# Performance work log

Hardware: AMD Instinct MI355X
Metric: run time of the kernel (lower is better)

## Reference

```python
import jax, jax.numpy as jnp
import numpy as np

# Gemma2-9B layer config
HID = 3584
H = 16          # query heads
KV = 8          # kv heads
G = H // KV     # GQA group size
DH = 256        # head dim
INTER = 14336
WINDOW = 1024   # sliding window size
LOGIT_CAP = 50.0
SCALING = 256.0 ** -0.5   # query_pre_attn_scalar ** -0.5
EPS = 1e-6
ROPE_BASE = 10000.0
B, S = 2, 2048


def gemma_rmsnorm(x, w, eps=EPS):
    # Gemma RMSNorm: fp32 compute, scale by (1 + w)
    xf = x.astype(jnp.float32)
    var = jnp.mean(xf * xf, axis=-1, keepdims=True)
    return (xf * jax.lax.rsqrt(var + eps) * (1.0 + w.astype(jnp.float32))).astype(x.dtype)


def apply_rope(pos, x):
    # neox-style rotary embedding; x: [B, S, n_heads, DH], pos: [B, S]
    half = DH // 2
    inv_freq = 1.0 / (ROPE_BASE ** (jnp.arange(0, half, dtype=jnp.float32) / half * 1.0))
    inv_freq = 1.0 / (ROPE_BASE ** (jnp.arange(0, DH, 2, dtype=jnp.float32) / DH))
    ang = pos.astype(jnp.float32)[..., None] * inv_freq          # [B, S, half]
    cos = jnp.cos(ang)[:, :, None, :]                            # [B, S, 1, half]
    sin = jnp.sin(ang)[:, :, None, :]
    x1, x2 = x[..., :half], x[..., half:]
    return jnp.concatenate([x1 * cos - x2 * sin, x2 * cos + x1 * sin], axis=-1).astype(x.dtype)


def setup_inputs() -> dict:
    key = jax.random.key(0)
    ks = jax.random.split(key, 12)
    s = 0.02
    inp = {
        "hidden_states": jax.random.normal(ks[0], (B, S, HID), dtype=jnp.float32),
        "positions": jnp.tile(jnp.arange(S, dtype=jnp.int32)[None, :], (B, 1)),
        "in_ln_w": jax.random.normal(ks[1], (HID,), dtype=jnp.float32) * s,
        "post_attn_ln_w": jax.random.normal(ks[2], (HID,), dtype=jnp.float32) * s,
        "pre_ff_ln_w": jax.random.normal(ks[3], (HID,), dtype=jnp.float32) * s,
        "post_ff_ln_w": jax.random.normal(ks[4], (HID,), dtype=jnp.float32) * s,
        "q_w": jax.random.normal(ks[5], (HID, H * DH), dtype=jnp.float32) * s,
        "k_w": jax.random.normal(ks[6], (HID, KV * DH), dtype=jnp.float32) * s,
        "v_w": jax.random.normal(ks[7], (HID, KV * DH), dtype=jnp.float32) * s,
        "o_w": jax.random.normal(ks[8], (H * DH, HID), dtype=jnp.float32) * s,
        "gate_w": jax.random.normal(ks[9], (HID, INTER), dtype=jnp.float32) * s,
        "up_w": jax.random.normal(ks[10], (HID, INTER), dtype=jnp.float32) * s,
        "down_w": jax.random.normal(ks[11], (INTER, HID), dtype=jnp.float32) * s,
    }
    return inp


def _decoder_layer(hidden_states, positions, in_ln_w, post_attn_ln_w, pre_ff_ln_w,
                   post_ff_ln_w, q_w, k_w, v_w, o_w, gate_w, up_w, down_w):
    # residual is None path
    residual = hidden_states
    x = gemma_rmsnorm(hidden_states, in_ln_w)

    # ---- attention ----
    q = (x @ q_w).reshape(B, S, H, DH)
    k = (x @ k_w).reshape(B, S, KV, DH)
    v = (x @ v_w).reshape(B, S, KV, DH)
    q = apply_rope(positions, q)
    k = apply_rope(positions, k)
    kv_fused = jnp.stack([k, v], axis=0)  # paged KV-cache write, modeled densely

    qg = q.reshape(B, S, KV, G, DH)
    # scores: [B, KV, G, S(q), S(k)]
    scores = jnp.einsum('bsngd,btnd->bngst', qg, k) * SCALING
    scores = LOGIT_CAP * jnp.tanh(scores / LOGIT_CAP)  # logit softcapping
    i = jnp.arange(S)[:, None]
    j = jnp.arange(S)[None, :]
    mask = (j <= i) & (i - j < WINDOW)                 # causal + sliding window
    scores = jnp.where(mask, scores, jnp.finfo(scores.dtype).min)
    probs = jax.nn.softmax(scores, axis=-1)
    attn = jnp.einsum('bngst,btnd->bsngd', probs, v).reshape(B, S, H * DH)
    attn_out = attn @ o_w

    x = gemma_rmsnorm(attn_out, post_attn_ln_w)
    x = residual + x
    residual = x

    # ---- GeGLU MLP ----
    x = gemma_rmsnorm(x, pre_ff_ln_w)
    inter = (x @ up_w) * jax.nn.gelu(x @ gate_w)
    x = inter @ down_w
    x = gemma_rmsnorm(x, post_ff_ln_w)
    return x, residual, kv_fused


def reference(hidden_states, positions, in_ln_w, post_attn_ln_w, pre_ff_ln_w,
              post_ff_ln_w, q_w, k_w, v_w, o_w, gate_w, up_w, down_w):
    return _decoder_layer(hidden_states, positions, in_ln_w, post_attn_ln_w,
                          pre_ff_ln_w, post_ff_ln_w, q_w, k_w, v_w, o_w,
                          gate_w, up_w, down_w)
```

## Files before the change

kernel.cpp:

```cpp
#include <hip/hip_runtime.h>
#include <stdint.h>

typedef unsigned short ushortT;
typedef float f32x4 __attribute__((ext_vector_type(4)));
typedef short short8 __attribute__((ext_vector_type(8)));

#define HID 3584
#define NH 16
#define NKV 8
#define DH 256
#define SEQ 2048
#define NB 2
#define NTOK 4096
#define INTERDIM 14336
#define WINDOW 1024

__device__ __forceinline__ ushortT f2bf(float x) {
  union { float f; uint32_t u; } v; v.f = x;
  uint32_t r = v.u + 0x7fffu + ((v.u >> 16) & 1u);
  return (ushortT)(r >> 16);
}
__device__ __forceinline__ float bf2f(uint32_t b) {
  union { uint32_t u; float f; } v; v.u = b << 16;
  return v.f;
}
__device__ __forceinline__ void gll16(const void* g, void* l) {
  __builtin_amdgcn_global_load_lds((const __attribute__((address_space(1))) void*)g,
                                   (__attribute__((address_space(3))) void*)l, 16, 0, 0);
}
__device__ __forceinline__ void sbar() {
  asm volatile("" ::: "memory");
  __builtin_amdgcn_s_barrier();
  asm volatile("" ::: "memory");
}
__device__ __forceinline__ void vmdrain() {
  asm volatile("s_waitcnt vmcnt(0)" ::: "memory");
}

__global__ __launch_bounds__(256) void transpose_cvt(const float* __restrict__ in,
                                                     ushortT* __restrict__ out,
                                                     int in_rs, int out_rs) {
  __shared__ float tile[64][65];
  const int r0 = blockIdx.y * 64, c0 = blockIdx.x * 64;
  const int t = threadIdx.x, tc = (t & 15) * 4, tr = t >> 4;
#pragma unroll
  for (int p = 0; p < 4; ++p) {
    int r = tr + p * 16;
    float4 v = *(const float4*)&in[(size_t)(r0 + r) * in_rs + c0 + tc];
    tile[r][tc] = v.x; tile[r][tc + 1] = v.y; tile[r][tc + 2] = v.z; tile[r][tc + 3] = v.w;
  }
  __syncthreads();
#pragma unroll
  for (int p = 0; p < 4; ++p) {
    int r = tr + p * 16;
    ushort4 u;
    u.x = f2bf(tile[tc + 0][r]); u.y = f2bf(tile[tc + 1][r]);
    u.z = f2bf(tile[tc + 2][r]); u.w = f2bf(tile[tc + 3][r]);
    *(ushort4*)&out[(size_t)(c0 + r) * out_rs + r0 + tc] = u;
  }
}

__global__ __launch_bounds__(256) void vtrans(const float* __restrict__ vsrc,
                                              ushortT* __restrict__ vT) {
  __shared__ float tile[64][65];
  const int z = blockIdx.z, b = z >> 3, n = z & 7;
  const float* in = vsrc + (size_t)b * SEQ * (NKV * DH) + n * DH;
  ushortT* out = vT + (size_t)z * DH * SEQ;
  const int s0 = blockIdx.y * 64, d0 = blockIdx.x * 64;
  const int t = threadIdx.x, tc = (t & 15) * 4, tr = t >> 4;
#pragma unroll
  for (int p = 0; p < 4; ++p) {
    int r = tr + p * 16;
    float4 v = *(const float4*)&in[(size_t)(s0 + r) * (NKV * DH) + d0 + tc];
    tile[r][tc] = v.x; tile[r][tc + 1] = v.y; tile[r][tc + 2] = v.z; tile[r][tc + 3] = v.w;
  }
  __syncthreads();
#pragma unroll
  for (int p = 0; p < 4; ++p) {
    int r = tr + p * 16;
    ushort4 u;
    u.x = f2bf(tile[tc + 0][r]); u.y = f2bf(tile[tc + 1][r]);
    u.z = f2bf(tile[tc + 2][r]); u.w = f2bf(tile[tc + 3][r]);
    *(ushort4*)&out[(size_t)(d0 + r) * SEQ + s0 + tc] = u;
  }
}

__device__ __forceinline__ float block_sum448(float v, float* sb) {
#pragma unroll
  for (int o = 32; o; o >>= 1) v += __shfl_xor(v, o, 64);
  __syncthreads();
  if ((threadIdx.x & 63) == 0) sb[threadIdx.x >> 6] = v;
  __syncthreads();
  float s = 0.f;
#pragma unroll
  for (int i = 0; i < 7; ++i) s += sb[i];
  return s;
}

__global__ __launch_bounds__(448) void rms_in(const float* __restrict__ in,
                                              const float* __restrict__ w,
                                              ushortT* __restrict__ out) {
  __shared__ float sb[8];
  const size_t row = blockIdx.x;
  const int c = threadIdx.x * 8;
  const float* p = in + row * HID + c;
  float4 a = *(const float4*)p, bq = *(const float4*)(p + 4);
  float v[8] = {a.x, a.y, a.z, a.w, bq.x, bq.y, bq.z, bq.w};
  float ssq = 0.f;
#pragma unroll
  for (int j = 0; j < 8; ++j) ssq += v[j] * v[j];
  float s = block_sum448(ssq, sb);
  float rs = rsqrtf(s * (1.0f / HID) + 1e-6f);
  uint32_t o[4];
#pragma unroll
  for (int j = 0; j < 4; ++j) {
    float r0 = v[2 * j] * rs * (1.f + w[c + 2 * j]);
    float r1 = v[2 * j + 1] * rs * (1.f + w[c + 2 * j + 1]);
    o[j] = (uint32_t)f2bf(r0) | ((uint32_t)f2bf(r1) << 16);
  }
  *(uint4*)(out + row * HID + c) = make_uint4(o[0], o[1], o[2], o[3]);
}

__global__ __launch_bounds__(448) void rms_add(const float* ao,
                                               const float* __restrict__ h,
                                               const float* __restrict__ w1,
                                               const float* __restrict__ w2,
                                               float* resid,
                                               ushortT* __restrict__ x2) {
  __shared__ float sb[8];
  const size_t row = blockIdx.x;
  const int c = threadIdx.x * 8;
  const float* p = ao + row * HID + c;
  float4 a = *(const float4*)p, bq = *(const float4*)(p + 4);
  float v[8] = {a.x, a.y, a.z, a.w, bq.x, bq.y, bq.z, bq.w};
  float ssq = 0.f;
#pragma unroll
  for (int j = 0; j < 8; ++j) ssq += v[j] * v[j];
  float s1 = block_sum448(ssq, sb);
  float rs1 = rsqrtf(s1 * (1.0f / HID) + 1e-6f);
  const float* hp = h + row * HID + c;
  float4 h0 = *(const float4*)hp, h1 = *(const float4*)(hp + 4);
  float hv[8] = {h0.x, h0.y, h0.z, h0.w, h1.x, h1.y, h1.z, h1.w};
  float r[8];
  float ssq2 = 0.f;
#pragma unroll
  for (int j = 0; j < 8; ++j) {
    r[j] = hv[j] + v[j] * rs1 * (1.f + w1[c + j]);
    ssq2 += r[j] * r[j];
  }
  float* rp = resid + row * HID + c;
  *(float4*)rp = make_float4(r[0], r[1], r[2], r[3]);
  *(float4*)(rp + 4) = make_float4(r[4], r[5], r[6], r[7]);
  float s2 = block_sum448(ssq2, sb);
  float rs2 = rsqrtf(s2 * (1.0f / HID) + 1e-6f);
  uint32_t o[4];
#pragma unroll
  for (int j = 0; j < 4; ++j) {
    float q0 = r[2 * j] * rs2 * (1.f + w2[c + 2 * j]);
    float q1 = r[2 * j + 1] * rs2 * (1.f + w2[c + 2 * j + 1]);
    o[j] = (uint32_t)f2bf(q0) | ((uint32_t)f2bf(q1) << 16);
  }
  *(uint4*)(x2 + row * HID + c) = make_uint4(o[0], o[1], o[2], o[3]);
}

__global__ __launch_bounds__(448) void rms_out(const float* in,
                                               const float* __restrict__ w,
                                               float* out) {
  __shared__ float sb[8];
  const size_t row = blockIdx.x;
  const int c = threadIdx.x * 8;
  const float* p = in + row * HID + c;
  float4 a = *(const float4*)p, bq = *(const float4*)(p + 4);
  float v[8] = {a.x, a.y, a.z, a.w, bq.x, bq.y, bq.z, bq.w};
  float ssq = 0.f;
#pragma unroll
  for (int j = 0; j < 8; ++j) ssq += v[j] * v[j];
  float s = block_sum448(ssq, sb);
  float rs = rsqrtf(s * (1.0f / HID) + 1e-6f);
  float* op = out + row * HID + c;
  float r[8];
#pragma unroll
  for (int j = 0; j < 8; ++j) r[j] = v[j] * rs * (1.f + w[c + j]);
  *(float4*)op = make_float4(r[0], r[1], r[2], r[3]);
  *(float4*)(op + 4) = make_float4(r[4], r[5], r[6], r[7]);
}

__global__ __launch_bounds__(128) void rope_q_k(const ushortT* __restrict__ qk,
                                                const int* __restrict__ pos,
                                                ushortT* __restrict__ qr) {
  const int s = blockIdx.x, h = blockIdx.y, b = blockIdx.z, i = threadIdx.x;
  float p = (float)pos[b * SEQ + s];
  float ang = p * exp2f(-(float)i * (13.287712379549449f / 128.f));
  float sn, cs;
  sincosf(ang, &sn, &cs);
  size_t ib = ((size_t)b * SEQ + s) * 6144 + (size_t)h * DH + i;
  float x1 = bf2f(qk[ib]), x2 = bf2f(qk[ib + 128]);
  size_t ob = (((size_t)b * NH + h) * SEQ + s) * DH + i;
  qr[ob] = f2bf(x1 * cs - x2 * sn);
  qr[ob + 128] = f2bf(x2 * cs + x1 * sn);
}

__global__ __launch_bounds__(128) void rope_k_k(const ushortT* __restrict__ qk,
                                                const int* __restrict__ pos,
                                                ushortT* __restrict__ kr,
                                                float* __restrict__ kv0) {
  const int s = blockIdx.x, n = blockIdx.y, b = blockIdx.z, i = threadIdx.x;
  float p = (float)pos[b * SEQ + s];
  float ang = p * exp2f(-(float)i * (13.287712379549449f / 128.f));
  float sn, cs;
  sincosf(ang, &sn, &cs);
  size_t ib = ((size_t)b * SEQ + s) * 6144 + 4096 + (size_t)n * DH + i;
  float x1 = bf2f(qk[ib]), x2 = bf2f(qk[ib + 128]);
  float o1 = x1 * cs - x2 * sn, o2 = x2 * cs + x1 * sn;
  size_t ob = (((size_t)b * NKV + n) * SEQ + s) * DH + i;
  kr[ob] = f2bf(o1);
  kr[ob + 128] = f2bf(o2);
  size_t kb = (((size_t)b * SEQ + s) * NKV + n) * DH + i;
  kv0[kb] = o1;
  kv0[kb + 128] = o2;
}

template <int OUTMODE>
__global__ __launch_bounds__(512) void gemm256(const ushortT* __restrict__ A, int lda,
                                               const ushortT* __restrict__ Bt, int ldb,
                                               void* C, const ushortT* G,
                                               int N, int K) {
  __shared__ ushortT lds[65536];
  char* lbase = (char*)lds;
  const int tid = threadIdx.x;
  const int nwg = gridDim.x * gridDim.y;
  const int lin = blockIdx.y * gridDim.x + blockIdx.x;
  const int cpx = nwg >> 3;
  const int lin2 = (lin & 7) * cpx + (lin >> 3);
  const int gy = gridDim.y;
  const int sq = lin2 / (gy * 16);
  const int rem = lin2 - sq * gy * 16;
  const int colq = rem / gy;
  const int bx = sq * 16 + colq;
  const int by = rem - colq * gy;
  const int m0 = by * 256, n0 = bx * 256;
  const int l = tid & 63, lr = l & 15, lg = l >> 4;
  const int wid = tid >> 6, wm2 = wid >> 2, wn4 = wid & 3;
  const int sr = tid >> 3, sc = tid & 7;

  f32x4 acc[8][4];
#pragma unroll
  for (int i = 0; i < 8; ++i)
#pragma unroll
    for (int j = 0; j < 4; ++j) acc[i][j] = (f32x4){0.f, 0.f, 0.f, 0.f};

  const int nt = K >> 6;
  const ushortT* Abase = A + (size_t)m0 * lda;
  const ushortT* Bbase = Bt + (size_t)n0 * ldb;

  auto stage_op = [&](const ushortT* gsrc, int ld, char* ldst) {
#pragma unroll
    for (int Li = 0; Li < 4; ++Li) {
      int r = Li * 64 + sr;
      gll16((const char*)(gsrc + (size_t)r * ld) + ((sc ^ (r & 7)) << 4),
            ldst + Li * 8192 + tid * 16);
    }
  };

  stage_op(Abase, lda, lbase);
  stage_op(Bbase, ldb, lbase + 32768);

  for (int t = 0; t < nt; ++t) {
    const int buf = t & 1;
    const char* Ab = lbase + buf * 65536 + wm2 * 16384;
    const char* Bb = lbase + buf * 65536 + 32768 + (wn4 >> 1) * 16384;
    short8 af[4][2], bfr[2][2];
#pragma unroll
    for (int q = 0; q < 4; ++q) {
      const int mh = q >> 1, nh = q & 1;
      if (q == 0) vmdrain();
      sbar();
      if (nh == 0) {
#pragma unroll
        for (int i = 0; i < 4; ++i) {
          int rA = mh * 64 + i * 16 + lr;
          int sw = rA & 7;
#pragma unroll
          for (int ks = 0; ks < 2; ++ks)
            af[i][ks] = *(const short8*)(Ab + rA * 128 + (((ks * 4 + lg) ^ sw) << 4));
        }
      }
#pragma unroll
      for (int j = 0; j < 2; ++j) {
        int rB = (wn4 & 1) * 64 + nh * 32 + j * 16 + lr;
        int sw = rB & 7;
#pragma unroll
        for (int ks = 0; ks < 2; ++ks)
          bfr[j][ks] = *(const short8*)(Bb + rB * 128 + (((ks * 4 + lg) ^ sw) << 4));
      }
      if (q == 0 && t + 1 < nt)
        stage_op(Abase + (size_t)(t + 1) * 64, lda, lbase + (buf ^ 1) * 65536);
      if (q == 1 && t + 1 < nt)
        stage_op(Bbase + (size_t)(t + 1) * 64, ldb, lbase + (buf ^ 1) * 65536 + 32768);
      __builtin_amdgcn_s_setprio(1);
#pragma unroll
      for (int i = 0; i < 4; ++i)
#pragma unroll
        for (int j = 0; j < 2; ++j)
#pragma unroll
          for (int ks = 0; ks < 2; ++ks)
            acc[mh * 4 + i][nh * 2 + j] = __builtin_amdgcn_mfma_f32_16x16x32_bf16(
                af[i][ks], bfr[j][ks], acc[mh * 4 + i][nh * 2 + j], 0, 0, 0);
      __builtin_amdgcn_s_setprio(0);
    }
  }
#pragma unroll
  for (int mi = 0; mi < 8; ++mi)
#pragma unroll
    for (int nj = 0; nj < 4; ++nj)
#pragma unroll
      for (int r = 0; r < 4; ++r) {
        size_t row = (size_t)(m0 + wm2 * 128 + mi * 16 + lg * 4 + r);
        size_t col = (size_t)(n0 + wn4 * 64 + nj * 16 + lr);
        size_t idx = row * N + col;
        if (OUTMODE == 0)
          ((float*)C)[idx] = acc[mi][nj][r];
        else if (OUTMODE == 1)
          ((ushortT*)C)[idx] = f2bf(acc[mi][nj][r]);
        else if (OUTMODE == 2)
          ((float*)C)[idx] += acc[mi][nj][r];
        else {
          float u = acc[mi][nj][r];
          float g = bf2f(G[idx]);
          float e = 0.5f * g * (1.f + tanhf(0.7978845608f * (g + 0.044715f * g * g * g)));
          ((ushortT*)C)[idx] = f2bf(u * e);
        }
      }
}

__global__ __launch_bounds__(256) void attn_fwd(const ushortT* __restrict__ Q,
                                                const ushortT* __restrict__ Kk,
                                                const ushortT* __restrict__ Vt,
                                                ushortT* __restrict__ Out) {
  __shared__ ushortT Kl[32 * 256];
  __shared__ ushortT Vl[256 * 32];
  __shared__ ushortT Pl[4][16 * 32];
  const int tid = threadIdx.x;
  const int w = tid >> 6, l = tid & 63, lr = l & 15, lg = l >> 4;
  const int h = blockIdx.y, b = blockIdx.z;
  const int n = h >> 1;
  const int qs = blockIdx.x * 64;
  const int sw = qs + w * 16;

  const ushortT* qp = Q + (((size_t)b * NH + h) * SEQ + (sw + lr)) * DH;
  short8 qf[8];
#pragma unroll
  for (int kk = 0; kk < 8; ++kk) qf[kk] = *(const short8*)(qp + kk * 32 + lg * 8);

  f32x4 acc[16];
#pragma unroll
  for (int i = 0; i < 16; ++i) acc[i] = (f32x4){0.f, 0.f, 0.f, 0.f};
  float m_s = -1e30f, l_s = 0.f;

  const ushortT* Kbase = Kk + ((size_t)b * NKV + n) * SEQ * DH;
  const ushortT* Vbase = Vt + ((size_t)b * NKV + n) * DH * SEQ;

  int tlo = qs - (WINDOW - 1);
  if (tlo < 0) tlo = 0;
  const int t0b = tlo & ~31;
  const int nt = (qs + 64 - t0b) >> 5;
  const int scol = sw + lr;

  for (int it = 0; it < nt; ++it) {
    const int t0 = t0b + it * 32;
    __syncthreads();
    {
      const int rowk = tid >> 5;
      const int cbk = (tid & 31) * 16;
#pragma unroll
      for (int c = 0; c < 4; ++c) {
        int row = c * 8 + rowk;
        int cbs = cbk ^ ((row & 7) << 4);
        gll16((const char*)(Kbase + (size_t)(t0 + row) * DH) + cbs, (char*)Kl + c * 4096 + tid * 16);
      }
      const int rowv = tid >> 2;
      const int cbv = (tid & 3) * 16;
#pragma unroll
      for (int c = 0; c < 4; ++c) {
        int row = c * 64 + rowv;
        int cbs = cbv ^ ((row & 3) << 4);
        gll16((const char*)(Vbase + (size_t)row * SEQ + t0) + cbs, (char*)Vl + c * 4096 + tid * 16);
      }
    }
    __syncthreads();
    f32x4 st[2];
#pragma unroll
    for (int tt = 0; tt < 2; ++tt) {
      f32x4 a = (f32x4){0.f, 0.f, 0.f, 0.f};
      const int krow = tt * 16 + lr;
      const char* kb = (const char*)Kl + krow * 512;
      const int swz = (krow & 7) << 4;
#pragma unroll
      for (int kk = 0; kk < 8; ++kk) {
        short8 kf = *(const short8*)(kb + ((kk * 64 + lg * 16) ^ swz));
        a = __builtin_amdgcn_mfma_f32_16x16x32_bf16(kf, qf[kk], a, 0, 0, 0);
      }
      st[tt] = a;
    }
    float pvv[8];
    float tmax = -1e30f;
#pragma unroll
    for (int tt = 0; tt < 2; ++tt)
#pragma unroll
      for (int r = 0; r < 4; ++r) {
        int t = t0 + tt * 16 + lg * 4 + r;
        float x = st[tt][r] * 0.0625f;
        x = 50.f * tanhf(x * 0.02f);
        bool ok = (t <= scol) && (scol - t < WINDOW);
        x = ok ? x : -1e30f;
        pvv[tt * 4 + r] = x;
        tmax = fmaxf(tmax, x);
      }
    tmax = fmaxf(tmax, __shfl_xor(tmax, 16, 64));
    tmax = fmaxf(tmax, __shfl_xor(tmax, 32, 64));
    float mnew = fmaxf(m_s, tmax);
    float fsc = __expf(m_s - mnew);
    m_s = mnew;
    float tsum = 0.f;
#pragma unroll
    for (int i = 0; i < 8; ++i) {
      pvv[i] = __expf(pvv[i] - mnew);
      tsum += pvv[i];
    }
    tsum += __shfl_xor(tsum, 16, 64);
    tsum += __shfl_xor(tsum, 32, 64);
    l_s = l_s * fsc + tsum;
    {
      char* pb = (char*)&Pl[w][0] + lr * 64;
      const int pswz = (lr & 3) << 4;
#pragma unroll
      for (int tt = 0; tt < 2; ++tt) {
        uint32_t p01 = (uint32_t)f2bf(pvv[tt * 4 + 0]) | ((uint32_t)f2bf(pvv[tt * 4 + 1]) << 16);
        uint32_t p23 = (uint32_t)f2bf(pvv[tt * 4 + 2]) | ((uint32_t)f2bf(pvv[tt * 4 + 3]) << 16);
        *(uint32_t*)(pb + ((tt * 32 + lg * 8 + 0) ^ pswz)) = p01;
        *(uint32_t*)(pb + ((tt * 32 + lg * 8 + 4) ^ pswz)) = p23;
      }
    }
    float fr[4];
#pragma unroll
    for (int r = 0; r < 4; ++r) fr[r] = __shfl(fsc, lg * 4 + r, 64);
#pragma unroll
    for (int nd = 0; nd < 16; ++nd) {
      acc[nd][0] *= fr[0]; acc[nd][1] *= fr[1];
      acc[nd][2] *= fr[2]; acc[nd][3] *= fr[3];
    }
    const char* pfb = (const char*)&Pl[w][0] + lr * 64;
    short8 pf = *(const short8*)(pfb + ((lg * 16) ^ ((lr & 3) << 4)));
#pragma unroll
    for (int nd = 0; nd < 16; ++nd) {
      const int vrow = nd * 16 + lr;
      short8 vf = *(const short8*)((const char*)Vl + vrow * 64 + ((lg * 16) ^ ((vrow & 3) << 4)));
      acc[nd] = __builtin_amdgcn_mfma_f32_16x16x32_bf16(pf, vf, acc[nd], 0, 0, 0);
    }
  }
  float linv[4];
#pragma unroll
  for (int r = 0; r < 4; ++r) linv[r] = 1.f / __shfl(l_s, lg * 4 + r, 64);
#pragma unroll
  for (int nd = 0; nd < 16; ++nd)
#pragma unroll
    for (int r = 0; r < 4; ++r) {
      size_t row = (size_t)b * SEQ + sw + lg * 4 + r;
      Out[row * (NH * DH) + (size_t)h * DH + nd * 16 + lr] = f2bf(acc[nd][r] * linv[r]);
    }
}

extern "C" void kernel_launch(void* const* d_in, const int* in_sizes, int n_in,
                              void* d_out, int out_size, void* d_ws, size_t ws_size,
                              hipStream_t stream) {
  const float* hs = (const float*)d_in[0];
  const int* pos = (const int*)d_in[1];
  const float* w_in = (const float*)d_in[2];
  const float* w_pa = (const float*)d_in[3];
  const float* w_pf = (const float*)d_in[4];
  const float* w_po = (const float*)d_in[5];
  const float* qw = (const float*)d_in[6];
  const float* kw = (const float*)d_in[7];
  const float* vw = (const float*)d_in[8];
  const float* ow = (const float*)d_in[9];
  const float* gw = (const float*)d_in[10];
  const float* uw = (const float*)d_in[11];
  const float* dw = (const float*)d_in[12];

  float* out_x = (float*)d_out;
  float* out_res = out_x + (size_t)NTOK * HID;
  float* out_kv0 = out_res + (size_t)NTOK * HID;
  float* out_kv1 = out_kv0 + (size_t)NTOK * NKV * DH;

  char* ws = (char*)d_ws;
  char* W = ws;
  ushortT* qwT = (ushortT*)(W);
  ushortT* kwT = (ushortT*)(W + 29360128);
  ushortT* vwT = (ushortT*)(W + 29360128 + 14680064);
  ushortT* owT = (ushortT*)(W + 29360128 + 2 * 14680064);
  ushortT* wF = (ushortT*)(W);
  char* R = ws + 102760448;
  ushortT* x1 = (ushortT*)(R);
  ushortT* qk_b = (ushortT*)(R + 29360128);
  ushortT* qrope = (ushortT*)(R + 79691776);
  ushortT* krope = (ushortT*)(R + 113246208);
  ushortT* vT = (ushortT*)(R + 130023424);
  ushortT* attnb = qk_b;
  ushortT* x2 = x1;
  ushortT* gateF = (ushortT*)(R + 29360128);
  ushortT* interF = gateF;
  float* attn_out = out_res;

  transpose_cvt<<<dim3(4096 / 64, HID / 64), 256, 0, stream>>>(qw, qwT, 4096, HID);
  transpose_cvt<<<dim3(2048 / 64, HID / 64), 256, 0, stream>>>(kw, kwT, 2048, HID);
  transpose_cvt<<<dim3(2048 / 64, HID / 64), 256, 0, stream>>>(vw, vwT, 2048, HID);
  transpose_cvt<<<dim3(HID / 64, 4096 / 64), 256, 0, stream>>>(ow, owT, HID, 4096);

  rms_in<<<NTOK, 448, 0, stream>>>(hs, w_in, x1);

  gemm256<1><<<dim3(24, 16), 512, 0, stream>>>(x1, HID, qwT, HID, qk_b, nullptr, 6144, HID);
  gemm256<0><<<dim3(8, 16), 512, 0, stream>>>(x1, HID, vwT, HID, out_kv1, nullptr, 2048, HID);

  rope_q_k<<<dim3(SEQ, NH, NB), 128, 0, stream>>>(qk_b, pos, qrope);
  rope_k_k<<<dim3(SEQ, NKV, NB), 128, 0, stream>>>(qk_b, pos, krope, out_kv0);
  vtrans<<<dim3(DH / 64, SEQ / 64, NB * NKV), 256, 0, stream>>>(out_kv1, vT);

  attn_fwd<<<dim3(SEQ / 64, NH, NB), 256, 0, stream>>>(qrope, krope, vT, attnb);

  gemm256<0><<<dim3(HID / 256, 16), 512, 0, stream>>>(attnb, 4096, owT, 4096, attn_out, nullptr,
                                                      HID, 4096);

  rms_add<<<NTOK, 448, 0, stream>>>(attn_out, hs, w_pa, w_pf, out_res, x2);

  transpose_cvt<<<dim3(INTERDIM / 64, HID / 64), 256, 0, stream>>>(gw, wF, INTERDIM, HID);
  gemm256<1><<<dim3(INTERDIM / 256, 16), 512, 0, stream>>>(x2, HID, wF, HID, gateF, nullptr,
                                                           INTERDIM, HID);
  transpose_cvt<<<dim3(INTERDIM / 64, HID / 64), 256, 0, stream>>>(uw, wF, INTERDIM, HID);
  gemm256<3><<<dim3(INTERDIM / 256, 16), 512, 0, stream>>>(x2, HID, wF, HID, interF, gateF,
                                                           INTERDIM, HID);
  transpose_cvt<<<dim3(HID / 64, INTERDIM / 64), 256, 0, stream>>>(dw, wF, HID, INTERDIM);
  gemm256<0><<<dim3(HID / 256, 16), 512, 0, stream>>>(interF, INTERDIM, wF, INTERDIM, out_x,
                                                      nullptr, HID, INTERDIM);

  rms_out<<<NTOK, 448, 0, stream>>>(out_x, w_po, out_x);
}
```

Baseline: 2.219 ms.

## Split MLP intermediate dimension into two chunks with accumulate-mode down GEMM

Processes the GeGLU MLP in two halves of the intermediate dimension. Each half transposes its gate, up and down weight slices, computes gate/inter for that slice, and runs the down projection, with the second pass accumulating into the output (gemm256<2>). This shrinks the intermediate activation and weight staging buffers so they may stay more cache-resident, at the cost of twice as many launches and smaller GEMM grids that may occupy the GPU less fully.

```diff
diff --git a/kernel.cpp b/kernel.cpp
--- a/kernel.cpp
+++ b/kernel.cpp
@@ -13,6 +13,7 @@
 #define NB 2
 #define NTOK 4096
 #define INTERDIM 14336
+#define ICH 7168
 #define WINDOW 1024
 
 __device__ __forceinline__ ushortT f2bf(float x) {
@@ -498,7 +499,8 @@
   ushortT* kwT = (ushortT*)(W + 29360128);
   ushortT* vwT = (ushortT*)(W + 29360128 + 14680064);
   ushortT* owT = (ushortT*)(W + 29360128 + 2 * 14680064);
-  ushortT* wF = (ushortT*)(W);
+  ushortT* wS0 = (ushortT*)(W);
+  ushortT* wS1 = (ushortT*)(W + 51380224);
   char* R = ws + 102760448;
   ushortT* x1 = (ushortT*)(R);
   ushortT* qk_b = (ushortT*)(R + 29360128);
@@ -507,8 +509,8 @@
   ushortT* vT = (ushortT*)(R + 130023424);
   ushortT* attnb = qk_b;
   ushortT* x2 = x1;
-  ushortT* gateF = (ushortT*)(R + 29360128);
-  ushortT* interF = gateF;
+  ushortT* gateC = (ushortT*)(R + 29360128);
+  ushortT* interC = gateC;
   float* attn_out = out_res;
 
   transpose_cvt<<<dim3(4096 / 64, HID / 64), 256, 0, stream>>>(qw, qwT, 4096, HID);
@@ -532,15 +534,24 @@
 
   rms_add<<<NTOK, 448, 0, stream>>>(attn_out, hs, w_pa, w_pf, out_res, x2);
 
-  transpose_cvt<<<dim3(INTERDIM / 64, HID / 64), 256, 0, stream>>>(gw, wF, INTERDIM, HID);
-  gemm256<1><<<dim3(INTERDIM / 256, 16), 512, 0, stream>>>(x2, HID, wF, HID, gateF, nullptr,
-                                                           INTERDIM, HID);
-  transpose_cvt<<<dim3(INTERDIM / 64, HID / 64), 256, 0, stream>>>(uw, wF, INTERDIM, HID);
-  gemm256<3><<<dim3(INTERDIM / 256, 16), 512, 0, stream>>>(x2, HID, wF, HID, interF, gateF,
-                                                           INTERDIM, HID);
-  transpose_cvt<<<dim3(HID / 64, INTERDIM / 64), 256, 0, stream>>>(dw, wF, HID, INTERDIM);
-  gemm256<0><<<dim3(HID / 256, 16), 512, 0, stream>>>(interF, INTERDIM, wF, INTERDIM, out_x,
-                                                      nullptr, HID, INTERDIM);
+  for (int c = 0; c < 2; ++c) {
+    transpose_cvt<<<dim3(ICH / 64, HID / 64), 256, 0, stream>>>(gw + (size_t)c * ICH, wS0,
+                                                                INTERDIM, HID);
+    gemm256<1><<<dim3(ICH / 256, 16), 512, 0, stream>>>(x2, HID, wS0, HID, gateC, nullptr,
+                                                        ICH, HID);
+    transpose_cvt<<<dim3(ICH / 64, HID / 64), 256, 0, stream>>>(uw + (size_t)c * ICH, wS1,
+                                                                INTERDIM, HID);
+    gemm256<3><<<dim3(ICH / 256, 16), 512, 0, stream>>>(x2, HID, wS1, HID, interC, gateC,
+                                                        ICH, HID);
+    transpose_cvt<<<dim3(HID / 64, ICH / 64), 256, 0, stream>>>(dw + (size_t)c * ICH * HID, wS0,
+                                                                HID, ICH);
+    if (c == 0)
+      gemm256<0><<<dim3(HID / 256, 16), 512, 0, stream>>>(interC, ICH, wS0, ICH, out_x, nullptr,
+                                                          HID, ICH);
+    else
+      gemm256<2><<<dim3(HID / 256, 16), 512, 0, stream>>>(interC, ICH, wS0, ICH, out_x, nullptr,
+                                                          HID, ICH);
+  }
 
   rms_out<<<NTOK, 448, 0, stream>>>(out_x, w_po, out_x);
 }
```

New measurement: 2.241 ms. About the same (+1.0%).
